# Performance work log

Hardware: AMD Instinct MI355X
Metric: run time of the kernel (lower is better)

Reference implementation:

```python
import jax, jax.numpy as jnp
import numpy as np

N = 100000   # nodes
E = 640000   # edges
D = 128      # init_node == hidden_node
L = 3        # layers (len('gcn_gcn_gcn'.split('_')))


def setup_inputs() -> dict:
    key = jax.random.key(0)
    ks = jax.random.split(key, 17)
    p = lambda k, shape: jax.random.normal(k, shape, jnp.float32) * 0.05
    return {
        "x": jax.random.normal(ks[0], (N, D), jnp.float32),
        "edge_attr": jax.random.uniform(ks[1], (E,), jnp.float32),
        "edge_index": jax.random.randint(ks[2], (2, E), 0, N),
        "conv_w": p(ks[3], (L, D, D)),       # SparseConv.weight
        "conv_lin_w": p(ks[4], (L, D, D)),   # SparseConv.lin (no bias)
        "l1_w": p(ks[5], (L, D, D)), "l1_b": p(ks[6], (L, D)),
        "l2_w": p(ks[7], (L, D, D)), "l2_b": p(ks[8], (L, D)),
        "mlp1_w": p(ks[9], (L, 2 * D, D)), "mlp1_b": p(ks[10], (L, D)),
        "mlp2_w": p(ks[11], (L, D, D)), "mlp2_b": p(ks[12], (L, D)),
        "post1_w": p(ks[13], (D, D)), "post1_b": p(ks[14], (D,)),
        "post2_w": p(ks[15], (D, D)), "post2_b": p(ks[16], (D,)),
    }


def reference(x, edge_attr, edge_index, conv_w, conv_lin_w,
              l1_w, l1_b, l2_w, l2_b, mlp1_w, mlp1_b, mlp2_w, mlp2_b,
              post1_w, post1_b, post2_w, post2_b):
    src, dst = edge_index[0], edge_index[1]  # PyG: message h_j from src, scatter-add at dst
    n = x.shape[0]

    def agg(h):
        # gather source features, weight per edge, scatter-add at targets
        return jax.ops.segment_sum(edge_attr[:, None] * h[src], dst, num_segments=n)

    mask = None
    for i in range(L):
        # --- WeightConv: computes sigmoid gate ---
        xm = x if mask is None else x * mask
        h = xm @ l1_w[i] + l1_b[i]
        w = jnp.concatenate([agg(h), xm @ l2_w[i] + l2_b[i]], axis=-1)  # [N, 2D]
        w = jax.nn.relu(jax.nn.relu(w) @ mlp1_w[i] + mlp1_b[i])
        mask = jax.nn.sigmoid(w @ mlp2_w[i] + mlp2_b[i])  # [N, D]
        # --- SparseConv: masked transform + propagate + residual lin ---
        h2 = (x * mask) @ conv_w[i]
        x = jax.nn.relu((agg(h2) + x @ conv_lin_w[i]) * mask)
    x = jax.nn.relu(x @ post1_w + post1_b)
    # F.dropout omitted (deterministic reference)
    return x @ post2_w + post2_b
```

## Files before the change

kernel.cpp:

```cpp
#include <hip/hip_runtime.h>
#include <math.h>

#define NN 100000
#define EE 640000
#define DD 128
#define NB_SCAN ((NN + 255) / 256)

typedef __attribute__((ext_vector_type(8))) short bf16x8;
typedef __attribute__((ext_vector_type(4))) float f32x4;

static __device__ __forceinline__ float4 ld4(const float* p) {
    return *reinterpret_cast<const float4*>(p);
}

static __device__ __forceinline__ unsigned short f2bf(float x) {
    unsigned u = __float_as_uint(x);
    return (unsigned short)((u + 0x7FFFu + ((u >> 16) & 1u)) >> 16);
}

static __device__ __forceinline__ void splitbf(float a, short& hi, short& lo) {
    unsigned u = __float_as_uint(a);
    unsigned hr = (u + 0x7FFFu + ((u >> 16) & 1u)) >> 16;
    float hf = __uint_as_float(hr << 16);
    float l = a - hf;
    unsigned ul = __float_as_uint(l);
    unsigned lr = (ul + 0x7FFFu + ((ul >> 16) & 1u)) >> 16;
    hi = (short)hr; lo = (short)lr;
}

__global__ void wfrag_k(const float* __restrict__ l1w, const float* __restrict__ l2w,
                        const float* __restrict__ mlp1w, const float* __restrict__ mlp2w,
                        const float* __restrict__ convw, const float* __restrict__ convlinw,
                        const float* __restrict__ post1w, const float* __restrict__ post2w,
                        unsigned short* __restrict__ Wh, unsigned short* __restrict__ Wl)
{
    const int b = blockIdx.x;
    const float* W; int slice; size_t fbase; int K;
    if (b < 12)      { W = l1w;      slice = b;      fbase = 0;      K = 128; }
    else if (b < 24) { W = l2w;      slice = b - 12; fbase = 49152;  K = 128; }
    else if (b < 48) { W = mlp1w;    slice = b - 24; fbase = 98304;  K = 256; }
    else if (b < 60) { W = mlp2w;    slice = b - 48; fbase = 196608; K = 128; }
    else if (b < 72) { W = convw;    slice = b - 60; fbase = 245760; K = 128; }
    else if (b < 84) { W = convlinw; slice = b - 72; fbase = 294912; K = 128; }
    else if (b < 88) { W = post1w;   slice = b - 84; fbase = 344064; K = 128; }
    else             { W = post2w;   slice = b - 88; fbase = 360448; K = 128; }
    const int kslices = K / 32;
    const int mat = slice / kslices;
    const int ks  = slice % kslices;
    const float* Wm = W + (size_t)mat * K * DD;
    const size_t outb = fbase + (size_t)mat * K * DD + (size_t)ks * 4096;
    const int t = threadIdx.x;
#pragma unroll
    for (int e = 0; e < 16; ++e) {
        const int f = t * 16 + e;
        const int r = f & 7, lane = (f >> 3) & 63, ct = f >> 9;
        const int krow = ks * 32 + (lane >> 4) * 8 + r;
        const int col  = ct * 16 + (lane & 15);
        short hh, ll;
        splitbf(Wm[(size_t)krow * DD + col], hh, ll);
        Wh[outb + f] = (unsigned short)hh; Wl[outb + f] = (unsigned short)ll;
    }
}

template<int KT, int DUAL, int RAW1, int MINW>
__launch_bounds__(256, MINW)
__global__ void gemm_f32A(const float* __restrict__ A,
                          const float* __restrict__ Amask,
                          const unsigned short* __restrict__ Wh0,
                          const unsigned short* __restrict__ Wl0,
                          const float* __restrict__ bias0, const int act0, const int obf0,
                          void* __restrict__ out0, const int ldo0, const int co0,
                          const unsigned short* __restrict__ Wh1,
                          const unsigned short* __restrict__ Wl1,
                          const float* __restrict__ bias1, const int obf1,
                          void* __restrict__ out1, const int ldo1, const int co1)
{
    __shared__ __align__(16) unsigned short Bs[16384];
    const int t = threadIdx.x, lane = t & 63, w = t >> 6;
    const int kg = lane >> 4, c16 = lane & 15;
    const int rb = blockIdx.x * 64 + w * 16;
    int ra = rb + c16; if (ra >= NN) ra = NN - 1;

    bf16x8 ah[KT], al[KT];
    bf16x8 uh[RAW1 ? KT : 1], ul[RAW1 ? KT : 1];
#pragma unroll
    for (int ks = 0; ks < KT; ++ks) {
        const float* ap = A + (size_t)ra * (KT * 32) + ks * 32 + kg * 8;
        const float4 v0 = ld4(ap), v1 = ld4(ap + 4);
        float tmp[8] = {v0.x, v0.y, v0.z, v0.w, v1.x, v1.y, v1.z, v1.w};
        if (RAW1) {
#pragma unroll
            for (int j = 0; j < 8; ++j) { short hh, ll; splitbf(tmp[j], hh, ll); uh[ks][j] = hh; ul[ks][j] = ll; }
        }
        if (Amask) {
            const float* mp = Amask + (size_t)ra * DD + ks * 32 + kg * 8;
            const float4 m0 = ld4(mp), m1 = ld4(mp + 4);
            tmp[0] *= m0.x; tmp[1] *= m0.y; tmp[2] *= m0.z; tmp[3] *= m0.w;
            tmp[4] *= m1.x; tmp[5] *= m1.y; tmp[6] *= m1.z; tmp[7] *= m1.w;
        }
#pragma unroll
        for (int j = 0; j < 8; ++j) { short hh, ll; splitbf(tmp[j], hh, ll); ah[ks][j] = hh; al[ks][j] = ll; }
    }

    auto pass = [&](const unsigned short* Wh, const unsigned short* Wl,
                    const bf16x8* xh, const bf16x8* xl,
                    const float* bias, const int act, const int obf,
                    void* out, const int ldo, const int co, const bool first) {
        f32x4 acc[8];
#pragma unroll
        for (int ct = 0; ct < 8; ++ct) acc[ct] = f32x4{0.f, 0.f, 0.f, 0.f};
#pragma unroll
        for (int st = 0; st < KT / 2; ++st) {
            if (!(first && st == 0)) __syncthreads();
#pragma unroll
            for (int i = 0; i < 4; ++i) {
                const int idx = i * 2048 + t * 8;
                *(uint4*)&Bs[idx]        = *(const uint4*)&Wh[(size_t)st * 8192 + idx];
                *(uint4*)&Bs[8192 + idx] = *(const uint4*)&Wl[(size_t)st * 8192 + idx];
            }
            __syncthreads();
#pragma unroll
            for (int s = 0; s < 2; ++s) {
                const int ks = st * 2 + s;
#pragma unroll
                for (int ct = 0; ct < 8; ++ct) {
                    const int fo = ((s * 8 + ct) * 64 + lane) * 8;
                    const bf16x8 bh = *(const bf16x8*)&Bs[fo];
                    const bf16x8 bl = *(const bf16x8*)&Bs[8192 + fo];
                    acc[ct] = __builtin_amdgcn_mfma_f32_16x16x32_bf16(xh[ks], bh, acc[ct], 0, 0, 0);
                    acc[ct] = __builtin_amdgcn_mfma_f32_16x16x32_bf16(xl[ks], bh, acc[ct], 0, 0, 0);
                    acc[ct] = __builtin_amdgcn_mfma_f32_16x16x32_bf16(xh[ks], bl, acc[ct], 0, 0, 0);
                }
            }
        }
#pragma unroll
        for (int ct = 0; ct < 8; ++ct) {
            const int c = ct * 16 + c16;
            const float b = bias ? bias[c] : 0.f;
#pragma unroll
            for (int r = 0; r < 4; ++r) {
                const int row = rb + kg * 4 + r;
                if (row < NN) {
                    float v = acc[ct][r] + b;
                    if (act == 1) v = fmaxf(v, 0.f);
                    if (obf) ((unsigned short*)out)[(size_t)row * ldo + co + c] = f2bf(v);
                    else     ((float*)out)[(size_t)row * ldo + co + c] = v;
                }
            }
        }
    };

    pass(Wh0, Wl0, ah, al, bias0, act0, obf0, out0, ldo0, co0, true);
    if (DUAL)
        pass(Wh1, Wl1, RAW1 ? uh : ah, RAW1 ? ul : al, bias1, 0, obf1, out1, ldo1, co1, false);
}

template<int KT, int MINW>
__launch_bounds__(256, MINW)
__global__ void gemm_bf16A(const unsigned short* __restrict__ A, const int reluA,
                           const unsigned short* __restrict__ Wh,
                           const unsigned short* __restrict__ Wl,
                           const float* __restrict__ bias, const int act, const int obf,
                           void* __restrict__ out, const int ldo, const int co)
{
    __shared__ __align__(16) unsigned short Bs[16384];
    const int t = threadIdx.x, lane = t & 63, w = t >> 6;
    const int kg = lane >> 4, c16 = lane & 15;
    const int rb = blockIdx.x * 64 + w * 16;
    int ra = rb + c16; if (ra >= NN) ra = NN - 1;

    bf16x8 ah[KT];
#pragma unroll
    for (int ks = 0; ks < KT; ++ks) {
        bf16x8 av = *(const bf16x8*)(A + (size_t)ra * (KT * 32) + ks * 32 + kg * 8);
        if (reluA) {
#pragma unroll
            for (int j = 0; j < 8; ++j) av[j] = (av[j] < 0) ? (short)0 : av[j];
        }
        ah[ks] = av;
    }

    f32x4 acc[8];
#pragma unroll
    for (int ct = 0; ct < 8; ++ct) acc[ct] = f32x4{0.f, 0.f, 0.f, 0.f};
#pragma unroll
    for (int st = 0; st < KT / 2; ++st) {
        if (st) __syncthreads();
#pragma unroll
        for (int i = 0; i < 4; ++i) {
            const int idx = i * 2048 + t * 8;
            *(uint4*)&Bs[idx]        = *(const uint4*)&Wh[(size_t)st * 8192 + idx];
            *(uint4*)&Bs[8192 + idx] = *(const uint4*)&Wl[(size_t)st * 8192 + idx];
        }
        __syncthreads();
#pragma unroll
        for (int s = 0; s < 2; ++s) {
            const int ks = st * 2 + s;
#pragma unroll
            for (int ct = 0; ct < 8; ++ct) {
                const int fo = ((s * 8 + ct) * 64 + lane) * 8;
                const bf16x8 bh = *(const bf16x8*)&Bs[fo];
                const bf16x8 bl = *(const bf16x8*)&Bs[8192 + fo];
                acc[ct] = __builtin_amdgcn_mfma_f32_16x16x32_bf16(ah[ks], bh, acc[ct], 0, 0, 0);
                acc[ct] = __builtin_amdgcn_mfma_f32_16x16x32_bf16(ah[ks], bl, acc[ct], 0, 0, 0);
            }
        }
    }
#pragma unroll
    for (int ct = 0; ct < 8; ++ct) {
        const int c = ct * 16 + c16;
        const float b = bias ? bias[c] : 0.f;
#pragma unroll
        for (int r = 0; r < 4; ++r) {
            const int row = rb + kg * 4 + r;
            if (row < NN) {
                float v = acc[ct][r] + b;
                if (act == 1) v = fmaxf(v, 0.f);
                else if (act == 2) v = 1.f / (1.f + __expf(-v));
                if (obf) ((unsigned short*)out)[(size_t)row * ldo + co + c] = f2bf(v);
                else     ((float*)out)[(size_t)row * ldo + co + c] = v;
            }
        }
    }
}

__launch_bounds__(256)
__global__ void spmm_bf16(const unsigned int* __restrict__ H2,
                          const int* __restrict__ rp,
                          const int* __restrict__ ccol,
                          const float* __restrict__ cval,
                          const float* __restrict__ addend,
                          const float* __restrict__ pmask,
                          const int act, const int obf,
                          float* __restrict__ outf, unsigned int* __restrict__ outb,
                          const int ldo)
{
    const int w = (blockIdx.x * 256 + threadIdx.x) >> 6;
    if (w >= NN) return;
    const int lane = threadIdx.x & 63;
    const int s = rp[w], e = rp[w + 1];
    float ax = 0.f, ay = 0.f;
    int j = s;
    while (j < e) {
        int cnt = e - j; if (cnt > 8) cnt = 8;
        int cols[8]; float vals[8];
#pragma unroll
        for (int q = 0; q < 8; ++q) {
            if (q < cnt) { cols[q] = ccol[j + q]; vals[q] = cval[j + q]; }
        }
#pragma unroll
        for (int q = 0; q < 8; ++q) {
            if (q < cnt) {
                const unsigned u = H2[(size_t)cols[q] * 64 + lane];
                ax = fmaf(vals[q], __uint_as_float(u << 16), ax);
                ay = fmaf(vals[q], __uint_as_float(u & 0xFFFF0000u), ay);
            }
        }
        j += cnt;
    }
    if (addend) {
        const float2 t = *reinterpret_cast<const float2*>(addend + (size_t)w * DD + lane * 2);
        ax += t.x; ay += t.y;
    }
    if (pmask) {
        const float2 m = *reinterpret_cast<const float2*>(pmask + (size_t)w * DD + lane * 2);
        ax *= m.x; ay *= m.y;
    }
    if (act == 1) { ax = fmaxf(ax, 0.f); ay = fmaxf(ay, 0.f); }
    if (obf) {
        outb[(size_t)w * ldo + lane] = (unsigned)f2bf(ax) | ((unsigned)f2bf(ay) << 16);
    } else {
        float2 o; o.x = ax; o.y = ay;
        *reinterpret_cast<float2*>(outf + (size_t)w * ldo + lane * 2) = o;
    }
}

__global__ void hist_k(const int* __restrict__ dstI, int* __restrict__ counts) {
    const int e = blockIdx.x * 256 + threadIdx.x;
    if (e < EE) atomicAdd(&counts[dstI[e]], 1);
}

__global__ void block_sums_k(const int* __restrict__ counts, int* __restrict__ bsum) {
    __shared__ int s[256];
    const int t = threadIdx.x;
    const int i = blockIdx.x * 256 + t;
    s[t] = (i < NN) ? counts[i] : 0;
    __syncthreads();
    for (int off = 128; off > 0; off >>= 1) {
        if (t < off) s[t] += s[t + off];
        __syncthreads();
    }
    if (t == 0) bsum[blockIdx.x] = s[0];
}

__global__ void scan_bsums_k(const int* __restrict__ bsum, int* __restrict__ bpre, const int nb) {
    __shared__ int s[512];
    const int t = threadIdx.x;
    s[t] = (t < nb) ? bsum[t] : 0;
    __syncthreads();
    for (int off = 1; off < 512; off <<= 1) {
        const int tmp = (t >= off) ? s[t - off] : 0;
        __syncthreads();
        s[t] += tmp;
        __syncthreads();
    }
    if (t < nb) bpre[t] = (t == 0) ? 0 : s[t - 1];
}

__global__ void scan_final_k(const int* __restrict__ counts, const int* __restrict__ bpre,
                             int* __restrict__ rowptr, int* __restrict__ nextc) {
    __shared__ int s[256];
    const int t = threadIdx.x;
    const int i = blockIdx.x * 256 + t;
    const int v = (i < NN) ? counts[i] : 0;
    s[t] = v;
    __syncthreads();
    for (int off = 1; off < 256; off <<= 1) {
        const int tmp = (t >= off) ? s[t - off] : 0;
        __syncthreads();
        s[t] += tmp;
        __syncthreads();
    }
    const int excl = s[t] - v + bpre[blockIdx.x];
    if (i < NN) { rowptr[i] = excl; nextc[i] = excl; }
    if (i == NN - 1) rowptr[NN] = EE;
}

__global__ void scatter_k(const int* __restrict__ srcI, const int* __restrict__ dstI,
                          const float* __restrict__ ea, int* __restrict__ nextc,
                          int* __restrict__ ccol, float* __restrict__ cval) {
    const int e = blockIdx.x * 256 + threadIdx.x;
    if (e >= EE) return;
    const int d = dstI[e];
    const int p = atomicAdd(&nextc[d], 1);
    ccol[p] = srcI[e];
    cval[p] = ea[e];
}

extern "C" void kernel_launch(void* const* d_in, const int* in_sizes, int n_in,
                              void* d_out, int out_size, void* d_ws, size_t ws_size,
                              hipStream_t stream)
{
    const float* x_in0      = (const float*)d_in[0];
    const float* edge_attr  = (const float*)d_in[1];
    const int*   edge_index = (const int*)d_in[2];
    const float* l1_b       = (const float*)d_in[6];
    const float* l2_b       = (const float*)d_in[8];
    const float* mlp1_b     = (const float*)d_in[10];
    const float* mlp2_b     = (const float*)d_in[12];
    const float* post1_b    = (const float*)d_in[14];
    const float* post2_b    = (const float*)d_in[16];

    const int* srcI = edge_index;
    const int* dstI = edge_index + EE;

    float* x_ws = (float*)d_out;

    float*          maskb  = (float*)d_ws;
    float*          tbuf   = maskb + (size_t)NN * DD;
    unsigned short* h16    = (unsigned short*)(tbuf + (size_t)NN * DD);
    unsigned short* cat16  = h16 + (size_t)NN * DD;
    unsigned short* gh16   = cat16 + (size_t)NN * 2 * DD;
    unsigned short* Wh_all = gh16 + (size_t)NN * DD;
    unsigned short* Wl_all = Wh_all + 376832;
    float* cval   = (float*)(Wl_all + 376832);
    int*   ccol   = (int*)(cval + EE);
    int*   rowptr = ccol + EE;
    int*   nextc  = rowptr + (NN + 1);
    int*   counts = nextc + NN;
    int*   bsum   = counts + NN;
    int*   bpre   = bsum + 512;

    wfrag_k<<<92, 256, 0, stream>>>((const float*)d_in[5], (const float*)d_in[7],
                                    (const float*)d_in[9], (const float*)d_in[11],
                                    (const float*)d_in[3], (const float*)d_in[4],
                                    (const float*)d_in[13], (const float*)d_in[15],
                                    Wh_all, Wl_all);
    hipMemsetAsync(counts, 0, NN * sizeof(int), stream);
    hist_k      <<<(EE + 255) / 256, 256, 0, stream>>>(dstI, counts);
    block_sums_k<<<NB_SCAN, 256, 0, stream>>>(counts, bsum);
    scan_bsums_k<<<1, 512, 0, stream>>>(bsum, bpre, NB_SCAN);
    scan_final_k<<<NB_SCAN, 256, 0, stream>>>(counts, bpre, rowptr, nextc);
    scatter_k   <<<(EE + 255) / 256, 256, 0, stream>>>(srcI, dstI, edge_attr, nextc, ccol, cval);

    const int GG = (NN + 63) / 64;
    const int SPMM_GRID = NN * 64 / 256;

    const size_t F_L1 = 0, F_L2 = 49152, F_M1 = 98304, F_M2 = 196608;
    const size_t F_CV = 245760, F_CL = 294912, F_P1 = 344064, F_P2 = 360448;

    for (int i = 0; i < 3; ++i) {
        const float* xc = (i == 0) ? x_in0 : x_ws;
        const float* pm = (i == 0) ? nullptr : maskb;
        const size_t o128 = (size_t)i * 16384, o256 = (size_t)i * 32768;
        gemm_f32A<4, 1, 0, 4><<<GG, 256, 0, stream>>>(xc, pm,
            Wh_all + F_L1 + o128, Wl_all + F_L1 + o128, l1_b + (size_t)i * DD, 0, 1, h16, DD, 0,
            Wh_all + F_L2 + o128, Wl_all + F_L2 + o128, l2_b + (size_t)i * DD, 1, cat16, 2 * DD, DD);
        spmm_bf16<<<SPMM_GRID, 256, 0, stream>>>((const unsigned*)h16, rowptr, ccol, cval,
            nullptr, nullptr, 0, 1, nullptr, (unsigned*)cat16, 2 * DD / 2);
        gemm_bf16A<8, 4><<<GG, 256, 0, stream>>>(cat16, 1,
            Wh_all + F_M1 + o256, Wl_all + F_M1 + o256, mlp1_b + (size_t)i * DD, 1, 1, gh16, DD, 0);
        gemm_bf16A<4, 4><<<GG, 256, 0, stream>>>(gh16, 0,
            Wh_all + F_M2 + o128, Wl_all + F_M2 + o128, mlp2_b + (size_t)i * DD, 2, 0, maskb, DD, 0);
        gemm_f32A<4, 1, 1, 3><<<GG, 256, 0, stream>>>(xc, maskb,
            Wh_all + F_CV + o128, Wl_all + F_CV + o128, nullptr, 0, 1, h16, DD, 0,
            Wh_all + F_CL + o128, Wl_all + F_CL + o128, nullptr, 0, tbuf, DD, 0);
        spmm_bf16<<<SPMM_GRID, 256, 0, stream>>>((const unsigned*)h16, rowptr, ccol, cval,
            tbuf, maskb, 1, 0, x_ws, nullptr, DD);
    }
    gemm_f32A<4, 0, 0, 4><<<GG, 256, 0, stream>>>(x_ws, nullptr,
        Wh_all + F_P1, Wl_all + F_P1, post1_b, 1, 1, gh16, DD, 0,
        nullptr, nullptr, nullptr, 0, nullptr, 0, 0);
    gemm_bf16A<4, 4><<<GG, 256, 0, stream>>>(gh16, 0,
        Wh_all + F_P2, Wl_all + F_P2, post2_b, 0, 0, (float*)d_out, DD, 0);

    (void)in_sizes; (void)n_in; (void)out_size; (void)ws_size;
}
```

Baseline: 1.187 ms.

## Use persistent GEMM kernels with resident LDS weights and vectorized epilogue stores

Replaces the 128-wide-K GEMMs with persistent kernels of 512 blocks. Each block loads the full hi/lo bf16 weight matrix into LDS once, then loops over 16-row tiles and prefetches the next tile's activations while computing. The weight fragment column layout is permuted so each lane holds 8 contiguous output columns, which allows 16-byte packed stores instead of scalar stores. The fused dual GEMMs are split into separate launches, which reads the input twice. Input splitting switches to truncation, and the gh16 buffer is dropped by reusing h16.

```diff
diff --git a/kernel.cpp b/kernel.cpp
--- a/kernel.cpp
+++ b/kernel.cpp
@@ -5,6 +5,9 @@
 #define EE 640000
 #define DD 128
 #define NB_SCAN ((NN + 255) / 256)
+#define NTILES 6250
+#define NBLK_R 512
+#define NWAVES_R (NBLK_R * 4)
 
 typedef __attribute__((ext_vector_type(8))) short bf16x8;
 typedef __attribute__((ext_vector_type(4))) float f32x4;
@@ -26,6 +29,13 @@
     unsigned ul = __float_as_uint(l);
     unsigned lr = (ul + 0x7FFFu + ((ul >> 16) & 1u)) >> 16;
     hi = (short)hr; lo = (short)lr;
+}
+
+static __device__ __forceinline__ void splitbf_t(float a, short& hi, short& lo) {
+    unsigned u = __float_as_uint(a);
+    hi = (short)(u >> 16);
+    float l = a - __uint_as_float(u & 0xFFFF0000u);
+    lo = (short)(__float_as_uint(l) >> 16);
 }
 
 __global__ void wfrag_k(const float* __restrict__ l1w, const float* __restrict__ l2w,
@@ -55,104 +65,205 @@
         const int f = t * 16 + e;
         const int r = f & 7, lane = (f >> 3) & 63, ct = f >> 9;
         const int krow = ks * 32 + (lane >> 4) * 8 + r;
-        const int col  = ct * 16 + (lane & 15);
+        const int col  = (lane & 15) * 8 + ct;
         short hh, ll;
         splitbf(Wm[(size_t)krow * DD + col], hh, ll);
         Wh[outb + f] = (unsigned short)hh; Wl[outb + f] = (unsigned short)ll;
     }
 }
 
-template<int KT, int DUAL, int RAW1, int MINW>
-__launch_bounds__(256, MINW)
-__global__ void gemm_f32A(const float* __restrict__ A,
+__launch_bounds__(256, 2)
+__global__ void gemmR_f32(const float* __restrict__ A,
                           const float* __restrict__ Amask,
-                          const unsigned short* __restrict__ Wh0,
-                          const unsigned short* __restrict__ Wl0,
-                          const float* __restrict__ bias0, const int act0, const int obf0,
-                          void* __restrict__ out0, const int ldo0, const int co0,
-                          const unsigned short* __restrict__ Wh1,
-                          const unsigned short* __restrict__ Wl1,
-                          const float* __restrict__ bias1, const int obf1,
-                          void* __restrict__ out1, const int ldo1, const int co1)
+                          const unsigned short* __restrict__ Wh,
+                          const unsigned short* __restrict__ Wl,
+                          const float* __restrict__ bias,
+                          const int act, const int obf,
+                          void* __restrict__ out, const int ldo, const int co)
 {
-    __shared__ __align__(16) unsigned short Bs[16384];
-    const int t = threadIdx.x, lane = t & 63, w = t >> 6;
+    __shared__ __align__(16) unsigned short Bs[32768];
+    const int t = threadIdx.x, lane = t & 63;
+#pragma unroll
+    for (int i = 0; i < 8; ++i) {
+        const int idx = i * 2048 + t * 8;
+        *(uint4*)&Bs[idx]         = *(const uint4*)&Wh[idx];
+        *(uint4*)&Bs[16384 + idx] = *(const uint4*)&Wl[idx];
+    }
+    __syncthreads();
+
     const int kg = lane >> 4, c16 = lane & 15;
-    const int rb = blockIdx.x * 64 + w * 16;
-    int ra = rb + c16; if (ra >= NN) ra = NN - 1;
-
-    bf16x8 ah[KT], al[KT];
-    bf16x8 uh[RAW1 ? KT : 1], ul[RAW1 ? KT : 1];
-#pragma unroll
-    for (int ks = 0; ks < KT; ++ks) {
-        const float* ap = A + (size_t)ra * (KT * 32) + ks * 32 + kg * 8;
-        const float4 v0 = ld4(ap), v1 = ld4(ap + 4);
-        float tmp[8] = {v0.x, v0.y, v0.z, v0.w, v1.x, v1.y, v1.z, v1.w};
-        if (RAW1) {
-#pragma unroll
-            for (int j = 0; j < 8; ++j) { short hh, ll; splitbf(tmp[j], hh, ll); uh[ks][j] = hh; ul[ks][j] = ll; }
-        }
+    float bv[8];
+    if (bias) {
+        const float4 b0 = ld4(bias + c16 * 8), b1 = ld4(bias + c16 * 8 + 4);
+        bv[0] = b0.x; bv[1] = b0.y; bv[2] = b0.z; bv[3] = b0.w;
+        bv[4] = b1.x; bv[5] = b1.y; bv[6] = b1.z; bv[7] = b1.w;
+    } else {
+#pragma unroll
+        for (int j = 0; j < 8; ++j) bv[j] = 0.f;
+    }
+
+    int tile = blockIdx.x * 4 + (t >> 6);
+    float4 cur[8];
+    if (tile < NTILES) {
+        const float* ap = A + (size_t)(tile * 16 + c16) * DD + kg * 8;
+#pragma unroll
+        for (int ks = 0; ks < 4; ++ks) { cur[2*ks] = ld4(ap + ks*32); cur[2*ks+1] = ld4(ap + ks*32 + 4); }
+    }
+    while (tile < NTILES) {
         if (Amask) {
-            const float* mp = Amask + (size_t)ra * DD + ks * 32 + kg * 8;
-            const float4 m0 = ld4(mp), m1 = ld4(mp + 4);
-            tmp[0] *= m0.x; tmp[1] *= m0.y; tmp[2] *= m0.z; tmp[3] *= m0.w;
-            tmp[4] *= m1.x; tmp[5] *= m1.y; tmp[6] *= m1.z; tmp[7] *= m1.w;
-        }
-#pragma unroll
-        for (int j = 0; j < 8; ++j) { short hh, ll; splitbf(tmp[j], hh, ll); ah[ks][j] = hh; al[ks][j] = ll; }
-    }
-
-    auto pass = [&](const unsigned short* Wh, const unsigned short* Wl,
-                    const bf16x8* xh, const bf16x8* xl,
-                    const float* bias, const int act, const int obf,
-                    void* out, const int ldo, const int co, const bool first) {
+            const float* mp = Amask + (size_t)(tile * 16 + c16) * DD + kg * 8;
+            float4 m[8];
+#pragma unroll
+            for (int ks = 0; ks < 4; ++ks) { m[2*ks] = ld4(mp + ks*32); m[2*ks+1] = ld4(mp + ks*32 + 4); }
+#pragma unroll
+            for (int q = 0; q < 8; ++q) {
+                cur[q].x *= m[q].x; cur[q].y *= m[q].y; cur[q].z *= m[q].z; cur[q].w *= m[q].w;
+            }
+        }
+        bf16x8 ah[4], al[4];
+#pragma unroll
+        for (int ks = 0; ks < 4; ++ks) {
+            const float e[8] = {cur[2*ks].x, cur[2*ks].y, cur[2*ks].z, cur[2*ks].w,
+                                cur[2*ks+1].x, cur[2*ks+1].y, cur[2*ks+1].z, cur[2*ks+1].w};
+#pragma unroll
+            for (int j = 0; j < 8; ++j) {
+                short hh, ll; splitbf_t(e[j], hh, ll);
+                ah[ks][j] = hh; al[ks][j] = ll;
+            }
+        }
+        const int ntile = tile + NWAVES_R;
+        if (ntile < NTILES) {
+            const float* ap = A + (size_t)(ntile * 16 + c16) * DD + kg * 8;
+#pragma unroll
+            for (int ks = 0; ks < 4; ++ks) { cur[2*ks] = ld4(ap + ks*32); cur[2*ks+1] = ld4(ap + ks*32 + 4); }
+        }
         f32x4 acc[8];
 #pragma unroll
         for (int ct = 0; ct < 8; ++ct) acc[ct] = f32x4{0.f, 0.f, 0.f, 0.f};
 #pragma unroll
-        for (int st = 0; st < KT / 2; ++st) {
-            if (!(first && st == 0)) __syncthreads();
-#pragma unroll
-            for (int i = 0; i < 4; ++i) {
-                const int idx = i * 2048 + t * 8;
-                *(uint4*)&Bs[idx]        = *(const uint4*)&Wh[(size_t)st * 8192 + idx];
-                *(uint4*)&Bs[8192 + idx] = *(const uint4*)&Wl[(size_t)st * 8192 + idx];
-            }
-            __syncthreads();
-#pragma unroll
-            for (int s = 0; s < 2; ++s) {
-                const int ks = st * 2 + s;
-#pragma unroll
-                for (int ct = 0; ct < 8; ++ct) {
-                    const int fo = ((s * 8 + ct) * 64 + lane) * 8;
-                    const bf16x8 bh = *(const bf16x8*)&Bs[fo];
-                    const bf16x8 bl = *(const bf16x8*)&Bs[8192 + fo];
-                    acc[ct] = __builtin_amdgcn_mfma_f32_16x16x32_bf16(xh[ks], bh, acc[ct], 0, 0, 0);
-                    acc[ct] = __builtin_amdgcn_mfma_f32_16x16x32_bf16(xl[ks], bh, acc[ct], 0, 0, 0);
-                    acc[ct] = __builtin_amdgcn_mfma_f32_16x16x32_bf16(xh[ks], bl, acc[ct], 0, 0, 0);
-                }
-            }
-        }
-#pragma unroll
-        for (int ct = 0; ct < 8; ++ct) {
-            const int c = ct * 16 + c16;
-            const float b = bias ? bias[c] : 0.f;
-#pragma unroll
-            for (int r = 0; r < 4; ++r) {
-                const int row = rb + kg * 4 + r;
-                if (row < NN) {
-                    float v = acc[ct][r] + b;
-                    if (act == 1) v = fmaxf(v, 0.f);
-                    if (obf) ((unsigned short*)out)[(size_t)row * ldo + co + c] = f2bf(v);
-                    else     ((float*)out)[(size_t)row * ldo + co + c] = v;
-                }
-            }
-        }
-    };
-
-    pass(Wh0, Wl0, ah, al, bias0, act0, obf0, out0, ldo0, co0, true);
-    if (DUAL)
-        pass(Wh1, Wl1, RAW1 ? uh : ah, RAW1 ? ul : al, bias1, 0, obf1, out1, ldo1, co1, false);
+        for (int ks = 0; ks < 4; ++ks) {
+#pragma unroll
+            for (int ct = 0; ct < 8; ++ct) {
+                const int fo = ((ks * 8 + ct) * 64 + lane) * 8;
+                const bf16x8 bh = *(const bf16x8*)&Bs[fo];
+                const bf16x8 bl = *(const bf16x8*)&Bs[16384 + fo];
+                acc[ct] = __builtin_amdgcn_mfma_f32_16x16x32_bf16(ah[ks], bh, acc[ct], 0, 0, 0);
+                acc[ct] = __builtin_amdgcn_mfma_f32_16x16x32_bf16(al[ks], bh, acc[ct], 0, 0, 0);
+                acc[ct] = __builtin_amdgcn_mfma_f32_16x16x32_bf16(ah[ks], bl, acc[ct], 0, 0, 0);
+            }
+        }
+#pragma unroll
+        for (int r = 0; r < 4; ++r) {
+            const int row = tile * 16 + kg * 4 + r;
+            float v[8];
+#pragma unroll
+            for (int ct = 0; ct < 8; ++ct) {
+                v[ct] = acc[ct][r] + bv[ct];
+                if (act == 1) v[ct] = fmaxf(v[ct], 0.f);
+                else if (act == 2) v[ct] = 1.f / (1.f + __expf(-v[ct]));
+            }
+            if (obf) {
+                uint4 pk;
+                pk.x = (unsigned)f2bf(v[0]) | ((unsigned)f2bf(v[1]) << 16);
+                pk.y = (unsigned)f2bf(v[2]) | ((unsigned)f2bf(v[3]) << 16);
+                pk.z = (unsigned)f2bf(v[4]) | ((unsigned)f2bf(v[5]) << 16);
+                pk.w = (unsigned)f2bf(v[6]) | ((unsigned)f2bf(v[7]) << 16);
+                *(uint4*)((unsigned short*)out + (size_t)row * ldo + co + c16 * 8) = pk;
+            } else {
+                float* op = (float*)out + (size_t)row * ldo + co + c16 * 8;
+                *(float4*)op       = make_float4(v[0], v[1], v[2], v[3]);
+                *(float4*)(op + 4) = make_float4(v[4], v[5], v[6], v[7]);
+            }
+        }
+        tile = ntile;
+    }
+}
+
+__launch_bounds__(256, 2)
+__global__ void gemmR_bf16(const unsigned short* __restrict__ A,
+                           const unsigned short* __restrict__ Wh,
+                           const unsigned short* __restrict__ Wl,
+                           const float* __restrict__ bias,
+                           const int act, const int obf,
+                           void* __restrict__ out, const int ldo, const int co)
+{
+    __shared__ __align__(16) unsigned short Bs[32768];
+    const int t = threadIdx.x, lane = t & 63;
+#pragma unroll
+    for (int i = 0; i < 8; ++i) {
+        const int idx = i * 2048 + t * 8;
+        *(uint4*)&Bs[idx]         = *(const uint4*)&Wh[idx];
+        *(uint4*)&Bs[16384 + idx] = *(const uint4*)&Wl[idx];
+    }
+    __syncthreads();
+
+    const int kg = lane >> 4, c16 = lane & 15;
+    float bv[8];
+    if (bias) {
+        const float4 b0 = ld4(bias + c16 * 8), b1 = ld4(bias + c16 * 8 + 4);
+        bv[0] = b0.x; bv[1] = b0.y; bv[2] = b0.z; bv[3] = b0.w;
+        bv[4] = b1.x; bv[5] = b1.y; bv[6] = b1.z; bv[7] = b1.w;
+    } else {
+#pragma unroll
+        for (int j = 0; j < 8; ++j) bv[j] = 0.f;
+    }
+
+    int tile = blockIdx.x * 4 + (t >> 6);
+    bf16x8 cur[4];
+    if (tile < NTILES) {
+        const unsigned short* ap = A + (size_t)(tile * 16 + c16) * DD + kg * 8;
+#pragma unroll
+        for (int ks = 0; ks < 4; ++ks) cur[ks] = *(const bf16x8*)(ap + ks * 32);
+    }
+    while (tile < NTILES) {
+        bf16x8 ah[4];
+#pragma unroll
+        for (int ks = 0; ks < 4; ++ks) ah[ks] = cur[ks];
+        const int ntile = tile + NWAVES_R;
+        if (ntile < NTILES) {
+            const unsigned short* ap = A + (size_t)(ntile * 16 + c16) * DD + kg * 8;
+#pragma unroll
+            for (int ks = 0; ks < 4; ++ks) cur[ks] = *(const bf16x8*)(ap + ks * 32);
+        }
+        f32x4 acc[8];
+#pragma unroll
+        for (int ct = 0; ct < 8; ++ct) acc[ct] = f32x4{0.f, 0.f, 0.f, 0.f};
+#pragma unroll
+        for (int ks = 0; ks < 4; ++ks) {
+#pragma unroll
+            for (int ct = 0; ct < 8; ++ct) {
+                const int fo = ((ks * 8 + ct) * 64 + lane) * 8;
+                const bf16x8 bh = *(const bf16x8*)&Bs[fo];
+                const bf16x8 bl = *(const bf16x8*)&Bs[16384 + fo];
+                acc[ct] = __builtin_amdgcn_mfma_f32_16x16x32_bf16(ah[ks], bh, acc[ct], 0, 0, 0);
+                acc[ct] = __builtin_amdgcn_mfma_f32_16x16x32_bf16(ah[ks], bl, acc[ct], 0, 0, 0);
+            }
+        }
+#pragma unroll
+        for (int r = 0; r < 4; ++r) {
+            const int row = tile * 16 + kg * 4 + r;
+            float v[8];
+#pragma unroll
+            for (int ct = 0; ct < 8; ++ct) {
+                v[ct] = acc[ct][r] + bv[ct];
+                if (act == 1) v[ct] = fmaxf(v[ct], 0.f);
+                else if (act == 2) v[ct] = 1.f / (1.f + __expf(-v[ct]));
+            }
+            if (obf) {
+                uint4 pk;
+                pk.x = (unsigned)f2bf(v[0]) | ((unsigned)f2bf(v[1]) << 16);
+                pk.y = (unsigned)f2bf(v[2]) | ((unsigned)f2bf(v[3]) << 16);
+                pk.z = (unsigned)f2bf(v[4]) | ((unsigned)f2bf(v[5]) << 16);
+                pk.w = (unsigned)f2bf(v[6]) | ((unsigned)f2bf(v[7]) << 16);
+                *(uint4*)((unsigned short*)out + (size_t)row * ldo + co + c16 * 8) = pk;
+            } else {
+                float* op = (float*)out + (size_t)row * ldo + co + c16 * 8;
+                *(float4*)op       = make_float4(v[0], v[1], v[2], v[3]);
+                *(float4*)(op + 4) = make_float4(v[4], v[5], v[6], v[7]);
+            }
+        }
+        tile = ntile;
+    }
 }
 
 template<int KT, int MINW>
@@ -179,6 +290,15 @@
         }
         ah[ks] = av;
     }
+    float bv[8];
+    if (bias) {
+        const float4 b0 = ld4(bias + c16 * 8), b1 = ld4(bias + c16 * 8 + 4);
+        bv[0] = b0.x; bv[1] = b0.y; bv[2] = b0.z; bv[3] = b0.w;
+        bv[4] = b1.x; bv[5] = b1.y; bv[6] = b1.z; bv[7] = b1.w;
+    } else {
+#pragma unroll
+        for (int j = 0; j < 8; ++j) bv[j] = 0.f;
+    }
 
     f32x4 acc[8];
 #pragma unroll
@@ -207,18 +327,27 @@
         }
     }
 #pragma unroll
-    for (int ct = 0; ct < 8; ++ct) {
-        const int c = ct * 16 + c16;
-        const float b = bias ? bias[c] : 0.f;
-#pragma unroll
-        for (int r = 0; r < 4; ++r) {
-            const int row = rb + kg * 4 + r;
-            if (row < NN) {
-                float v = acc[ct][r] + b;
-                if (act == 1) v = fmaxf(v, 0.f);
-                else if (act == 2) v = 1.f / (1.f + __expf(-v));
-                if (obf) ((unsigned short*)out)[(size_t)row * ldo + co + c] = f2bf(v);
-                else     ((float*)out)[(size_t)row * ldo + co + c] = v;
+    for (int r = 0; r < 4; ++r) {
+        const int row = rb + kg * 4 + r;
+        if (row < NN) {
+            float v[8];
+#pragma unroll
+            for (int ct = 0; ct < 8; ++ct) {
+                v[ct] = acc[ct][r] + bv[ct];
+                if (act == 1) v[ct] = fmaxf(v[ct], 0.f);
+                else if (act == 2) v[ct] = 1.f / (1.f + __expf(-v[ct]));
+            }
+            if (obf) {
+                uint4 pk;
+                pk.x = (unsigned)f2bf(v[0]) | ((unsigned)f2bf(v[1]) << 16);
+                pk.y = (unsigned)f2bf(v[2]) | ((unsigned)f2bf(v[3]) << 16);
+                pk.z = (unsigned)f2bf(v[4]) | ((unsigned)f2bf(v[5]) << 16);
+                pk.w = (unsigned)f2bf(v[6]) | ((unsigned)f2bf(v[7]) << 16);
+                *(uint4*)((unsigned short*)out + (size_t)row * ldo + co + c16 * 8) = pk;
+            } else {
+                float* op = (float*)out + (size_t)row * ldo + co + c16 * 8;
+                *(float4*)op       = make_float4(v[0], v[1], v[2], v[3]);
+                *(float4*)(op + 4) = make_float4(v[4], v[5], v[6], v[7]);
             }
         }
     }
@@ -360,8 +489,7 @@
     float*          tbuf   = maskb + (size_t)NN * DD;
     unsigned short* h16    = (unsigned short*)(tbuf + (size_t)NN * DD);
     unsigned short* cat16  = h16 + (size_t)NN * DD;
-    unsigned short* gh16   = cat16 + (size_t)NN * 2 * DD;
-    unsigned short* Wh_all = gh16 + (size_t)NN * DD;
+    unsigned short* Wh_all = cat16 + (size_t)NN * 2 * DD;
     unsigned short* Wl_all = Wh_all + 376832;
     float* cval   = (float*)(Wl_all + 376832);
     int*   ccol   = (int*)(cval + EE);
@@ -393,25 +521,29 @@
         const float* xc = (i == 0) ? x_in0 : x_ws;
         const float* pm = (i == 0) ? nullptr : maskb;
         const size_t o128 = (size_t)i * 16384, o256 = (size_t)i * 32768;
-        gemm_f32A<4, 1, 0, 4><<<GG, 256, 0, stream>>>(xc, pm,
-            Wh_all + F_L1 + o128, Wl_all + F_L1 + o128, l1_b + (size_t)i * DD, 0, 1, h16, DD, 0,
-            Wh_all + F_L2 + o128, Wl_all + F_L2 + o128, l2_b + (size_t)i * DD, 1, cat16, 2 * DD, DD);
+        gemmR_f32<<<NBLK_R, 256, 0, stream>>>(xc, pm,
+            Wh_all + F_L1 + o128, Wl_all + F_L1 + o128, l1_b + (size_t)i * DD,
+            0, 1, h16, DD, 0);
+        gemmR_f32<<<NBLK_R, 256, 0, stream>>>(xc, pm,
+            Wh_all + F_L2 + o128, Wl_all + F_L2 + o128, l2_b + (size_t)i * DD,
+            0, 1, cat16, 2 * DD, DD);
         spmm_bf16<<<SPMM_GRID, 256, 0, stream>>>((const unsigned*)h16, rowptr, ccol, cval,
             nullptr, nullptr, 0, 1, nullptr, (unsigned*)cat16, 2 * DD / 2);
         gemm_bf16A<8, 4><<<GG, 256, 0, stream>>>(cat16, 1,
-            Wh_all + F_M1 + o256, Wl_all + F_M1 + o256, mlp1_b + (size_t)i * DD, 1, 1, gh16, DD, 0);
-        gemm_bf16A<4, 4><<<GG, 256, 0, stream>>>(gh16, 0,
-            Wh_all + F_M2 + o128, Wl_all + F_M2 + o128, mlp2_b + (size_t)i * DD, 2, 0, maskb, DD, 0);
-        gemm_f32A<4, 1, 1, 3><<<GG, 256, 0, stream>>>(xc, maskb,
-            Wh_all + F_CV + o128, Wl_all + F_CV + o128, nullptr, 0, 1, h16, DD, 0,
-            Wh_all + F_CL + o128, Wl_all + F_CL + o128, nullptr, 0, tbuf, DD, 0);
+            Wh_all + F_M1 + o256, Wl_all + F_M1 + o256, mlp1_b + (size_t)i * DD, 1, 1, h16, DD, 0);
+        gemmR_bf16<<<NBLK_R, 256, 0, stream>>>(h16,
+            Wh_all + F_M2 + o128, Wl_all + F_M2 + o128, mlp2_b + (size_t)i * DD,
+            2, 0, maskb, DD, 0);
+        gemmR_f32<<<NBLK_R, 256, 0, stream>>>(xc, maskb,
+            Wh_all + F_CV + o128, Wl_all + F_CV + o128, nullptr, 0, 1, h16, DD, 0);
+        gemmR_f32<<<NBLK_R, 256, 0, stream>>>(xc, nullptr,
+            Wh_all + F_CL + o128, Wl_all + F_CL + o128, nullptr, 0, 0, tbuf, DD, 0);
         spmm_bf16<<<SPMM_GRID, 256, 0, stream>>>((const unsigned*)h16, rowptr, ccol, cval,
             tbuf, maskb, 1, 0, x_ws, nullptr, DD);
     }
-    gemm_f32A<4, 0, 0, 4><<<GG, 256, 0, stream>>>(x_ws, nullptr,
-        Wh_all + F_P1, Wl_all + F_P1, post1_b, 1, 1, gh16, DD, 0,
-        nullptr, nullptr, nullptr, 0, nullptr, 0, 0);
-    gemm_bf16A<4, 4><<<GG, 256, 0, stream>>>(gh16, 0,
+    gemmR_f32<<<NBLK_R, 256, 0, stream>>>(x_ws, nullptr,
+        Wh_all + F_P1, Wl_all + F_P1, post1_b, 1, 1, h16, DD, 0);
+    gemmR_bf16<<<NBLK_R, 256, 0, stream>>>(h16,
         Wh_all + F_P2, Wl_all + F_P2, post2_b, 0, 0, (float*)d_out, DD, 0);
 
     (void)in_sizes; (void)n_in; (void)out_size; (void)ws_size;
```

After: 1.855 ms. +56.3%, slower.
